# Performance work log

Hardware: AMD Instinct MI355X
Metric: run time of the kernel (lower is better)

The kernel has to match this reference:

```python
import jax, jax.numpy as jnp
import numpy as np

H = 16   # nheads
WIN = 64 # window_size (= sqrt(n) so the b,h,n//w,n//w,dk view is valid)


def setup_inputs() -> dict:
    key = jax.random.key(0)
    ks = jax.random.split(key, 7)
    b, n, d = 4, 4096, 1024
    q = jax.random.normal(ks[0], (b, n, d), dtype=jnp.float32)
    k = jax.random.normal(ks[1], (b, n, d), dtype=jnp.float32)
    v = jax.random.normal(ks[2], (b, n, d), dtype=jnp.float32)
    # nn.Linear(d, d, bias=False) weights, stored torch-style as (out, in)
    Wq = jax.random.normal(ks[3], (d, d), dtype=jnp.float32) * 0.02
    Wk = jax.random.normal(ks[4], (d, d), dtype=jnp.float32) * 0.02
    Wv = jax.random.normal(ks[5], (d, d), dtype=jnp.float32) * 0.02
    Wo = jax.random.normal(ks[6], (d, d), dtype=jnp.float32) * 0.02
    return {"q": q, "k": k, "v": v, "Wq": Wq, "Wk": Wk, "Wv": Wv, "Wo": Wo, "window": 1}


def _attention(q, k, v, Wq, Wk, Wv, Wo, window):
    b, qn, d = q.shape
    n = k.shape[1]
    dk = d // H
    # torch Linear: x @ W.T
    qh = (q @ Wq.T).reshape(b, qn, H, dk).transpose(0, 2, 1, 3)  # (b,h,qn,dk)
    kh = (k @ Wk.T).reshape(b, n, H, dk).transpose(0, 2, 1, 3)
    vh = (v @ Wv.T).reshape(b, n, H, dk).transpose(0, 2, 1, 3)
    if window and WIN > 0:
        nw = n // WIN  # requires n == nw*nw, as in the torch .view
        qh = qh.reshape(b, H, nw, nw, dk)
        kh = kh.reshape(b, H, nw, nw, dk)
        vh = vh.reshape(b, H, nw, nw, dk)
    scale = jnp.float32(1.0) / jnp.sqrt(jnp.float32(dk))
    attn = jnp.einsum('...qd,...kd->...qk', qh, kh) * scale  # block-local scores
    attn = jax.nn.softmax(attn, axis=-1)
    o = jnp.einsum('...qk,...kd->...qd', attn, vh)
    # torch: attn.transpose(1, -2).contiguous().view(b, qn, d)
    o = jnp.swapaxes(o, 1, -2).reshape(b, qn, d)
    return o @ Wo.T


def reference(q, k, v, Wq, Wk, Wv, Wo, window):
    return _attention(q, k, v, Wq, Wk, Wv, Wo, window)
```

## Files before the change

kernel.cpp:

```cpp
#include <hip/hip_runtime.h>


typedef unsigned short u16;
typedef unsigned int u32;
typedef __bf16 bf16x8 __attribute__((ext_vector_type(8)));
typedef float f32x4 __attribute__((ext_vector_type(4)));
typedef u16 u16x8 __attribute__((ext_vector_type(8)));

__device__ __forceinline__ u16 f2bf(float f) {
  u32 u = __builtin_bit_cast(u32, f);
  u += 0x7fffu + ((u >> 16) & 1u);
  return (u16)(u >> 16);
}

__device__ __forceinline__ void cvt8_store(const float* __restrict__ src,
                                           u16* __restrict__ dst, size_t i) {
  const float4 a = *(const float4*)(src + i);
  const float4 b = *(const float4*)(src + i + 4);
  u16x8 r;
  r[0] = f2bf(a.x); r[1] = f2bf(a.y); r[2] = f2bf(a.z); r[3] = f2bf(a.w);
  r[4] = f2bf(b.x); r[5] = f2bf(b.y); r[6] = f2bf(b.z); r[7] = f2bf(b.w);
  *(u16x8*)(dst + i) = r;
}

__global__ __launch_bounds__(256) void cvt_kernel(const float* __restrict__ src,
                                                  u16* __restrict__ dst) {
  cvt8_store(src, dst, ((size_t)blockIdx.x * 256 + threadIdx.x) * 8);
}

__global__ __launch_bounds__(256) void cvtw_kernel(
    const float* __restrict__ Wq, const float* __restrict__ Wk,
    const float* __restrict__ Wv, const float* __restrict__ Wo,
    u16* __restrict__ dst) {
  const float* src = (blockIdx.z == 0) ? Wq : (blockIdx.z == 1) ? Wk
                   : (blockIdx.z == 2) ? Wv : Wo;
  cvt8_store(src, dst + (size_t)blockIdx.z * 1048576,
             ((size_t)blockIdx.x * 256 + threadIdx.x) * 8);
}

__device__ __forceinline__ void cp16(const u16* g, u16* l) {
  __builtin_amdgcn_global_load_lds((const __attribute__((address_space(1))) void*)g,
                                   (__attribute__((address_space(3))) void*)l, 16, 0, 0);
}

__global__ __launch_bounds__(256, 2) void gemm_bt_kernel(
    const u16* __restrict__ A, const u16* __restrict__ B, void* __restrict__ Cv,
    int cf) {
  constexpr int N = 1024, K = 1024;
  __shared__ u16 lA[128 * 32];
  __shared__ u16 lB[128 * 32];
  const int tid = threadIdx.x;
  const int lane = tid & 63, w = tid >> 6;
  const int quad = lane >> 4, lr = lane & 15;
  const int m0 = blockIdx.y * 128, n0 = blockIdx.x * 128;
  const int wr = (w >> 1) * 64, wc = (w & 1) * 64;

  const int ch1 = tid, ch2 = tid + 256;
  const u16* Ag1 = A + (size_t)(m0 + (ch1 >> 2)) * K + (ch1 & 3) * 8;
  const u16* Ag2 = A + (size_t)(m0 + (ch2 >> 2)) * K + (ch2 & 3) * 8;
  const u16* Bg1 = B + (size_t)(n0 + (ch1 >> 2)) * K + (ch1 & 3) * 8;
  const u16* Bg2 = B + (size_t)(n0 + (ch2 >> 2)) * K + (ch2 & 3) * 8;

  f32x4 acc[4][4] = {};
  for (int k0 = 0; k0 < K; k0 += 32) {
    cp16(Ag1 + k0, &lA[ch1 * 8]);
    cp16(Ag2 + k0, &lA[ch2 * 8]);
    cp16(Bg1 + k0, &lB[ch1 * 8]);
    cp16(Bg2 + k0, &lB[ch2 * 8]);
    __syncthreads();
    bf16x8 afr[4], bfr[4];
#pragma unroll
    for (int mi = 0; mi < 4; ++mi)
      afr[mi] = *(const bf16x8*)&lA[(wr + mi * 16 + lr) * 32 + quad * 8];
#pragma unroll
    for (int ni = 0; ni < 4; ++ni)
      bfr[ni] = *(const bf16x8*)&lB[(wc + ni * 16 + lr) * 32 + quad * 8];
#pragma unroll
    for (int mi = 0; mi < 4; ++mi)
#pragma unroll
      for (int ni = 0; ni < 4; ++ni)
        acc[mi][ni] = __builtin_amdgcn_mfma_f32_16x16x32_bf16(afr[mi], bfr[ni], acc[mi][ni], 0, 0, 0);
    __syncthreads();
  }
#pragma unroll
  for (int mi = 0; mi < 4; ++mi)
#pragma unroll
    for (int r = 0; r < 4; ++r) {
      const int row = m0 + wr + mi * 16 + quad * 4 + r;
      if (!cf) {
        u16* dst = (u16*)Cv + (size_t)row * N + n0 + wc + lr;
#pragma unroll
        for (int ni = 0; ni < 4; ++ni) dst[ni * 16] = f2bf(acc[mi][ni][r]);
      } else {
        float* dst = (float*)Cv + (size_t)row * N + n0 + wc + lr;
#pragma unroll
        for (int ni = 0; ni < 4; ++ni) dst[ni * 16] = acc[mi][ni][r];
      }
    }
}

__global__ __launch_bounds__(64) void attn_win_kernel(
    const u16* __restrict__ Xq, const u16* __restrict__ Xk, const u16* __restrict__ Xv,
    u16* __restrict__ Xo) {
  __shared__ u16 P[64 * 72];
  __shared__ u16 VT[64 * 72];
  const int bx = blockIdx.x;
  const int wi = bx & 63, h = (bx >> 6) & 15, b = bx >> 10;
  const int lane = threadIdx.x & 63, quad = lane >> 4, lr = lane & 15;
  const size_t tb = (size_t)b * 4096 + wi * 64;
  const u16* qb = Xq + tb * 1024 + h * 64;
  const u16* kb = Xk + tb * 1024 + h * 64;
  const u16* vb = Xv + tb * 1024 + h * 64;

  bf16x8 aq[4][2], bk[4][2];
#pragma unroll
  for (int mi = 0; mi < 4; ++mi)
#pragma unroll
    for (int ks = 0; ks < 2; ++ks) {
      aq[mi][ks] = *(const bf16x8*)(qb + (size_t)(mi * 16 + lr) * 1024 + ks * 32 + quad * 8);
      bk[mi][ks] = *(const bf16x8*)(kb + (size_t)(mi * 16 + lr) * 1024 + ks * 32 + quad * 8);
    }
  f32x4 s[4][4];
#pragma unroll
  for (int mi = 0; mi < 4; ++mi)
#pragma unroll
    for (int ni = 0; ni < 4; ++ni) {
      f32x4 z = {0.f, 0.f, 0.f, 0.f};
      z = __builtin_amdgcn_mfma_f32_16x16x32_bf16(aq[mi][0], bk[ni][0], z, 0, 0, 0);
      s[mi][ni] = __builtin_amdgcn_mfma_f32_16x16x32_bf16(aq[mi][1], bk[ni][1], z, 0, 0, 0);
    }

  const float sc = 0.125f;
#pragma unroll
  for (int mi = 0; mi < 4; ++mi)
#pragma unroll
    for (int r = 0; r < 4; ++r) {
      float mx = fmaxf(fmaxf(s[mi][0][r], s[mi][1][r]), fmaxf(s[mi][2][r], s[mi][3][r]));
#pragma unroll
      for (int m = 1; m < 16; m <<= 1) mx = fmaxf(mx, __shfl_xor(mx, m));
      float sum = 0.f;
#pragma unroll
      for (int ni = 0; ni < 4; ++ni) {
        float p = __expf((s[mi][ni][r] - mx) * sc);
        s[mi][ni][r] = p;
        sum += p;
      }
#pragma unroll
      for (int m = 1; m < 16; m <<= 1) sum += __shfl_xor(sum, m);
      const float inv = 1.f / sum;
#pragma unroll
      for (int ni = 0; ni < 4; ++ni) s[mi][ni][r] *= inv;
    }

#pragma unroll
  for (int mi = 0; mi < 4; ++mi)
#pragma unroll
    for (int ni = 0; ni < 4; ++ni)
#pragma unroll
      for (int r = 0; r < 4; ++r)
        P[(mi * 16 + quad * 4 + r) * 72 + ni * 16 + lr] = f2bf(s[mi][ni][r]);

  {
    const u16* vr = vb + (size_t)lane * 1024;
#pragma unroll
    for (int j = 0; j < 64; j += 8) {
      u16x8 t = *(const u16x8*)(vr + j);
#pragma unroll
      for (int jj = 0; jj < 8; ++jj) VT[(j + jj) * 72 + lane] = t[jj];
    }
  }
  __syncthreads();

  f32x4 o[4][4] = {};
#pragma unroll
  for (int ks = 0; ks < 2; ++ks) {
    bf16x8 ap[4], bv[4];
#pragma unroll
    for (int mi = 0; mi < 4; ++mi)
      ap[mi] = *(const bf16x8*)&P[(mi * 16 + lr) * 72 + ks * 32 + quad * 8];
#pragma unroll
    for (int ci = 0; ci < 4; ++ci)
      bv[ci] = *(const bf16x8*)&VT[(ci * 16 + lr) * 72 + ks * 32 + quad * 8];
#pragma unroll
    for (int mi = 0; mi < 4; ++mi)
#pragma unroll
      for (int ci = 0; ci < 4; ++ci)
        o[mi][ci] = __builtin_amdgcn_mfma_f32_16x16x32_bf16(ap[mi], bv[ci], o[mi][ci], 0, 0, 0);
  }

#pragma unroll
  for (int mi = 0; mi < 4; ++mi)
#pragma unroll
    for (int r = 0; r < 4; ++r) {
      const int qp = mi * 16 + quad * 4 + r;
      u16* dst = Xo + ((size_t)b * 4096 + (size_t)qp * 64 + wi) * 1024 + h * 64 + lr;
#pragma unroll
      for (int ci = 0; ci < 4; ++ci) dst[ci * 16] = f2bf(o[mi][ci][r]);
    }
}

extern "C" void kernel_launch(void* const* d_in, const int* in_sizes, int n_in,
                              void* d_out, int out_size, void* d_ws, size_t ws_size,
                              hipStream_t stream) {
  (void)in_sizes; (void)n_in; (void)out_size; (void)ws_size;
  const float* q  = (const float*)d_in[0];
  const float* k  = (const float*)d_in[1];
  const float* v  = (const float*)d_in[2];
  const float* Wq = (const float*)d_in[3];
  const float* Wk = (const float*)d_in[4];
  const float* Wv = (const float*)d_in[5];
  const float* Wo = (const float*)d_in[6];

  constexpr size_t ELEMS = (size_t)16384 * 1024;
  u16* Xq = (u16*)d_out;
  u16* qb = (u16*)d_out + ELEMS;
  u16* Wb = (u16*)d_in[0];
  u16* S1 = (u16*)d_ws;
  u16* Xk = S1 + ELEMS;
  u16* Xv = Xk + ELEMS;
  u16* Xo = S1;

  cvt_kernel<<<8192, 256, 0, stream>>>(q, qb);
  cvtw_kernel<<<dim3(512, 1, 4), 256, 0, stream>>>(Wq, Wk, Wv, Wo, Wb);
  cvt_kernel<<<8192, 256, 0, stream>>>(k, S1);
  gemm_bt_kernel<<<dim3(8, 128), 256, 0, stream>>>(qb, Wb, Xq, 0);
  gemm_bt_kernel<<<dim3(8, 128), 256, 0, stream>>>(S1, Wb + 1048576, Xk, 0);
  cvt_kernel<<<8192, 256, 0, stream>>>(v, S1);
  gemm_bt_kernel<<<dim3(8, 128), 256, 0, stream>>>(S1, Wb + 2097152, Xv, 0);
  attn_win_kernel<<<dim3(4096), 64, 0, stream>>>(Xq, Xk, Xv, Xo);
  gemm_bt_kernel<<<dim3(8, 128), 256, 0, stream>>>(Xo, Wb + 3145728, (float*)d_out, 1);
}
```

Baseline: 452.6 us.

## Remap GEMM blocks per XCD and load V fragments directly into registers

The GEMM launch moves to a 1D grid, and block IDs are remapped so that consecutive blocks on each of the 8 XCDs cover contiguous M rows and share A tiles in that XCD's L2. In the attention kernel, the V transpose through shared memory is removed. Each lane now gathers its MFMA B-operand fragment straight from global memory with strided scalar 16-bit loads, saving LDS space and scatter stores. The cost is many uncoalesced 2-byte global loads in place of vector loads.

Result: faster. 432.3 us (-4.5%).

```diff
diff --git a/kernel.cpp b/kernel.cpp
--- a/kernel.cpp
+++ b/kernel.cpp
@@ -52,7 +52,10 @@
   const int tid = threadIdx.x;
   const int lane = tid & 63, w = tid >> 6;
   const int quad = lane >> 4, lr = lane & 15;
-  const int m0 = blockIdx.y * 128, n0 = blockIdx.x * 128;
+  const int lid = blockIdx.x;
+  const int xcd = lid & 7, slot = lid >> 3;
+  const int m0 = (xcd * 16 + (slot >> 3)) * 128;
+  const int n0 = (slot & 7) * 128;
   const int wr = (w >> 1) * 64, wc = (w & 1) * 64;
 
   const int ch1 = tid, ch2 = tid + 256;
@@ -103,7 +106,6 @@
     const u16* __restrict__ Xq, const u16* __restrict__ Xk, const u16* __restrict__ Xv,
     u16* __restrict__ Xo) {
   __shared__ u16 P[64 * 72];
-  __shared__ u16 VT[64 * 72];
   const int bx = blockIdx.x;
   const int wi = bx & 63, h = (bx >> 6) & 15, b = bx >> 10;
   const int lane = threadIdx.x & 63, quad = lane >> 4, lr = lane & 15;
@@ -130,6 +132,16 @@
       s[mi][ni] = __builtin_amdgcn_mfma_f32_16x16x32_bf16(aq[mi][1], bk[ni][1], z, 0, 0, 0);
     }
 
+  u16x8 bvr[2][4];
+#pragma unroll
+  for (int ks = 0; ks < 2; ++ks)
+#pragma unroll
+    for (int ci = 0; ci < 4; ++ci) {
+      const u16* vc = vb + (size_t)(ks * 32 + quad * 8) * 1024 + ci * 16 + lr;
+#pragma unroll
+      for (int j = 0; j < 8; ++j) bvr[ks][ci][j] = vc[(size_t)j * 1024];
+    }
+
   const float sc = 0.125f;
 #pragma unroll
   for (int mi = 0; mi < 4; ++mi)
@@ -159,33 +171,21 @@
 #pragma unroll
       for (int r = 0; r < 4; ++r)
         P[(mi * 16 + quad * 4 + r) * 72 + ni * 16 + lr] = f2bf(s[mi][ni][r]);
-
-  {
-    const u16* vr = vb + (size_t)lane * 1024;
-#pragma unroll
-    for (int j = 0; j < 64; j += 8) {
-      u16x8 t = *(const u16x8*)(vr + j);
-#pragma unroll
-      for (int jj = 0; jj < 8; ++jj) VT[(j + jj) * 72 + lane] = t[jj];
-    }
-  }
   __syncthreads();
 
   f32x4 o[4][4] = {};
 #pragma unroll
   for (int ks = 0; ks < 2; ++ks) {
-    bf16x8 ap[4], bv[4];
+    bf16x8 ap[4];
 #pragma unroll
     for (int mi = 0; mi < 4; ++mi)
       ap[mi] = *(const bf16x8*)&P[(mi * 16 + lr) * 72 + ks * 32 + quad * 8];
 #pragma unroll
-    for (int ci = 0; ci < 4; ++ci)
-      bv[ci] = *(const bf16x8*)&VT[(ci * 16 + lr) * 72 + ks * 32 + quad * 8];
-#pragma unroll
     for (int mi = 0; mi < 4; ++mi)
 #pragma unroll
       for (int ci = 0; ci < 4; ++ci)
-        o[mi][ci] = __builtin_amdgcn_mfma_f32_16x16x32_bf16(ap[mi], bv[ci], o[mi][ci], 0, 0, 0);
+        o[mi][ci] = __builtin_amdgcn_mfma_f32_16x16x32_bf16(
+            ap[mi], __builtin_bit_cast(bf16x8, bvr[ks][ci]), o[mi][ci], 0, 0, 0);
   }
 
 #pragma unroll
@@ -223,10 +223,10 @@
   cvt_kernel<<<8192, 256, 0, stream>>>(q, qb);
   cvtw_kernel<<<dim3(512, 1, 4), 256, 0, stream>>>(Wq, Wk, Wv, Wo, Wb);
   cvt_kernel<<<8192, 256, 0, stream>>>(k, S1);
-  gemm_bt_kernel<<<dim3(8, 128), 256, 0, stream>>>(qb, Wb, Xq, 0);
-  gemm_bt_kernel<<<dim3(8, 128), 256, 0, stream>>>(S1, Wb + 1048576, Xk, 0);
+  gemm_bt_kernel<<<1024, 256, 0, stream>>>(qb, Wb, Xq, 0);
+  gemm_bt_kernel<<<1024, 256, 0, stream>>>(S1, Wb + 1048576, Xk, 0);
   cvt_kernel<<<8192, 256, 0, stream>>>(v, S1);
-  gemm_bt_kernel<<<dim3(8, 128), 256, 0, stream>>>(S1, Wb + 2097152, Xv, 0);
+  gemm_bt_kernel<<<1024, 256, 0, stream>>>(S1, Wb + 2097152, Xv, 0);
   attn_win_kernel<<<dim3(4096), 64, 0, stream>>>(Xq, Xk, Xv, Xo);
-  gemm_bt_kernel<<<dim3(8, 128), 256, 0, stream>>>(Xo, Wb + 3145728, (float*)d_out, 1);
-}
+  gemm_bt_kernel<<<1024, 256, 0, stream>>>(Xo, Wb + 3145728, (float*)d_out, 1);
+}
```
